# Kernel tuning notes

Hardware: AMD Instinct MI355X
Metric: run time of the kernel (lower is better)

Reference implementation:

```python
import jax, jax.numpy as jnp
import numpy as np

N_NODES = 50000
N_EDGES = 800000
HEADS = 2
HID = 64
NEG_SLOPE = 0.2


def setup_inputs() -> dict:
    key = jax.random.key(0)
    ks = jax.random.split(key, 8)
    x = jax.random.normal(ks[0], (N_NODES, 128), dtype=jnp.float32)
    W_src = jax.random.normal(ks[1], (128, HEADS * HID), dtype=jnp.float32) * (1.0 / np.sqrt(128))
    W_dst = jax.random.normal(ks[2], (128, HEADS * HID), dtype=jnp.float32) * (1.0 / np.sqrt(128))
    att_src = jax.random.normal(ks[3], (HEADS, HID), dtype=jnp.float32) * 0.1
    att_dst = jax.random.normal(ks[4], (HEADS, HID), dtype=jnp.float32) * 0.1
    bias = jax.random.normal(ks[5], (HEADS * HID,), dtype=jnp.float32) * 0.01
    prelu_w = jnp.full((HEADS * HID,), 0.25, dtype=jnp.float32)
    edge_index = jax.random.randint(ks[6], (2, N_EDGES), 0, N_NODES, dtype=jnp.int64)
    return {"x": x, "W_src": W_src, "W_dst": W_dst, "att_src": att_src,
            "att_dst": att_dst, "bias": bias, "prelu_w": prelu_w,
            "edge_index": edge_index}


def gat_prelu(x, W_src, W_dst, att_src, att_dst, bias, prelu_w, edge_index):
    N = x.shape[0]
    src, dst = edge_index[0], edge_index[1]
    xs = (x @ W_src).reshape(N, HEADS, HID)   # [N,H,C]
    xd = (x @ W_dst).reshape(N, HEADS, HID)
    a_src = jnp.einsum('nhc,hc->nh', xs, att_src)  # [N,H]
    a_dst = jnp.einsum('nhc,hc->nh', xd, att_dst)
    e = jax.nn.leaky_relu(a_src[src] + a_dst[dst], NEG_SLOPE)  # [E,H]
    # segment softmax over incoming edges of each dst node
    m = jax.ops.segment_max(e, dst, num_segments=N)            # [N,H]
    ee = jnp.exp(e - m[dst])
    denom = jax.ops.segment_sum(ee, dst, num_segments=N)
    alpha = ee / (denom[dst] + 1e-16)                          # [E,H]
    msg = xs[src] * alpha[:, :, None]                          # [E,H,C]
    out = jax.ops.segment_sum(msg, dst, num_segments=N)        # [N,H,C]
    out = out.reshape(N, HEADS * HID) + bias
    return jnp.where(out >= 0, out, prelu_w * out)


def reference(x, W_src, W_dst, att_src, att_dst, bias, prelu_w, edge_index):
    return gat_prelu(x, W_src, W_dst, att_src, att_dst, bias, prelu_w, edge_index)
```

## Files before the change

kernel.cpp:

```cpp
#include <hip/hip_runtime.h>
#include <hip/hip_fp16.h>


#define N_NODES 50000
#define N_EDGES 800000
#define CAP     56
#define BSH     8
#define NB      196
#define CHUNK   4096
#define NBLK    196
#define CCAP    64

#define OFF_A      0
#define OFF_CNT    800000
#define OFF_XS     1000256
#define OFF_BKT    13800256
#define OFF_SWZ    36200256
#define DOUT_COARSE 0
#define DOUT_CELL   19668992

typedef _Float16 f16x8 __attribute__((ext_vector_type(8)));
typedef float    f32x4 __attribute__((ext_vector_type(4)));
typedef unsigned long long u64;

__global__ __launch_bounds__(256) void k0_prep(
    const float* __restrict__ Wsrc, const float* __restrict__ Wdst,
    const float* __restrict__ att_s, const float* __restrict__ att_d,
    __half* __restrict__ swz)
{
    __shared__ float vS[128 * 4];
    const int nt = blockIdx.x;
    const int t = threadIdx.x;
    if (nt == 8) {
        if (t < 128) {
            const float* wsp = Wsrc + t * 128;
            const float* wdp = Wdst + t * 128;
            float a0 = 0.f, a1 = 0.f, a2 = 0.f, a3 = 0.f;
#pragma unroll 8
            for (int c = 0; c < 64; ++c) {
                a0 += wsp[c]      * att_s[c];
                a1 += wsp[64 + c] * att_s[64 + c];
                a2 += wdp[c]      * att_d[c];
                a3 += wdp[64 + c] * att_d[64 + c];
            }
            *(float4*)(vS + t * 4) = make_float4(a0, a1, a2, a3);
        }
        __syncthreads();
    }
    const int kb = t >> 6, L = t & 63;
    const int col = L & 15;
    const int krow = kb * 32 + ((L >> 4) & 3) * 8;
    f16x8 v;
    if (nt < 8) {
#pragma unroll
        for (int j = 0; j < 8; ++j)
            v[j] = (_Float16)Wsrc[(size_t)(krow + j) * 128 + nt * 16 + col];
    } else {
#pragma unroll
        for (int j = 0; j < 8; ++j)
            v[j] = (col < 4) ? (_Float16)vS[(krow + j) * 4 + col] : (_Float16)0.f;
    }
    *(f16x8*)(swz + ((size_t)(kb * 9 + nt) * 64 + L) * 8) = v;
}

__global__ __launch_bounds__(256) void k1_gemm(
    const float* __restrict__ x, const __half* __restrict__ swz,
    __half* __restrict__ xs, float* __restrict__ a_all)
{
    __shared__ __half tile[64 * 136];
    const int t = threadIdx.x;
    const int w = t >> 6, L = t & 63;
    const int m = L & 15, q = L >> 4;
    const int n_a = blockIdx.x * 64 + w * 16 + m;
    const int rrow = (n_a < N_NODES) ? n_a : (N_NODES - 1);
    const float* xrow = x + (size_t)rrow * 128;

    f32x4 acc[9];
#pragma unroll
    for (int nt = 0; nt < 9; ++nt) acc[nt] = (f32x4){0.f, 0.f, 0.f, 0.f};

#pragma unroll
    for (int kb = 0; kb < 4; ++kb) {
        const int k0 = kb * 32 + q * 8;
        float4 xa = *(const float4*)(xrow + k0);
        float4 xb = *(const float4*)(xrow + k0 + 4);
        f16x8 a;
        a[0] = (_Float16)xa.x; a[1] = (_Float16)xa.y;
        a[2] = (_Float16)xa.z; a[3] = (_Float16)xa.w;
        a[4] = (_Float16)xb.x; a[5] = (_Float16)xb.y;
        a[6] = (_Float16)xb.z; a[7] = (_Float16)xb.w;
        const f16x8* bbase = (const f16x8*)swz + (size_t)(kb * 9) * 64 + L;
#pragma unroll
        for (int nt = 0; nt < 9; ++nt) {
            f16x8 b = bbase[(size_t)nt * 64];
            acc[nt] = __builtin_amdgcn_mfma_f32_16x16x32_f16(a, b, acc[nt], 0, 0, 0);
        }
    }

    const int rloc = w * 16 + q * 4;
#pragma unroll
    for (int nt = 0; nt < 8; ++nt) {
#pragma unroll
        for (int r = 0; r < 4; ++r)
            tile[(rloc + r) * 136 + nt * 16 + m] = (__half)acc[nt][r];
    }
    __syncthreads();
    const int n0 = blockIdx.x * 64;
#pragma unroll
    for (int cc = 0; cc < 4; ++cc) {
        int task = cc * 256 + t;
        int row = task >> 4, ch = (task & 15) * 8;
        int n = n0 + row;
        if (n < N_NODES) {
            ulonglong2 v = *(const ulonglong2*)(tile + row * 136 + ch);
            *(ulonglong2*)(xs + (size_t)n * 128 + ch) = v;
        }
    }

    if (m < 4) {
#pragma unroll
        for (int r = 0; r < 4; ++r) {
            int n = n0 + rloc + r;
            if (n < N_NODES) a_all[(size_t)n * 4 + m] = acc[8][r];
        }
    }
}

__global__ __launch_bounds__(256) void kB_bin(
    const int* __restrict__ ei, const float* __restrict__ a_all,
    u64* __restrict__ coarse, int* __restrict__ cellcnt)
{
    __shared__ int lcnt[NB];
    const int t = threadIdx.x;
    if (t < NB) lcnt[t] = 0;
    __syncthreads();
    const int e0 = blockIdx.x * CHUNK;
#pragma unroll
    for (int u = 0; u < 8; ++u) {
        int e = e0 + u * 512 + t * 2;
        if (e < N_EDGES) {
            int2 ss = *(const int2*)(ei + e);
            int2 dd = *(const int2*)(ei + N_EDGES + e);
            float2 as0 = *(const float2*)(a_all + (size_t)ss.x * 4);
            float2 ad0 = *(const float2*)(a_all + (size_t)dd.x * 4 + 2);
            float2 as1 = *(const float2*)(a_all + (size_t)ss.y * 4);
            float2 ad1 = *(const float2*)(a_all + (size_t)dd.y * 4 + 2);
            float e00 = as0.x + ad0.x, e01 = as0.y + ad0.y;
            float e10 = as1.x + ad1.x, e11 = as1.y + ad1.y;
            e00 = (e00 >= 0.f) ? e00 : 0.2f * e00;
            e01 = (e01 >= 0.f) ? e01 : 0.2f * e01;
            e10 = (e10 >= 0.f) ? e10 : 0.2f * e10;
            e11 = (e11 >= 0.f) ? e11 : 0.2f * e11;
            __half2 hw0 = __floats2half2_rn(__expf(e00), __expf(e01));
            __half2 hw1 = __floats2half2_rn(__expf(e10), __expf(e11));
            unsigned lo0 = (unsigned)ss.x | ((unsigned)(dd.x & 255) << 16);
            unsigned lo1 = (unsigned)ss.y | ((unsigned)(dd.y & 255) << 16);
            u64 ent0 = (u64)lo0 | ((u64)*reinterpret_cast<unsigned*>(&hw0) << 32);
            u64 ent1 = (u64)lo1 | ((u64)*reinterpret_cast<unsigned*>(&hw1) << 32);
            int b0 = dd.x >> BSH, b1 = dd.y >> BSH;
            int p0 = atomicAdd(&lcnt[b0], 1);
            int p1 = atomicAdd(&lcnt[b1], 1);
            if (p0 < CCAP)
                coarse[((size_t)b0 * NBLK + blockIdx.x) * CCAP + p0] = ent0;
            if (p1 < CCAP)
                coarse[((size_t)b1 * NBLK + blockIdx.x) * CCAP + p1] = ent1;
        }
    }
    __syncthreads();
    if (t < NB) {
        int c = lcnt[t];
        cellcnt[t * NBLK + blockIdx.x] = (c < CCAP) ? c : CCAP;
    }
}

__global__ __launch_bounds__(512) void kD_fine(
    const u64* __restrict__ coarse, const int* __restrict__ cellcnt,
    int* __restrict__ cnt, int2* __restrict__ bkt)
{
    __shared__ int cur[256];
    __shared__ int ccnt[NBLK];
    const int b = blockIdx.x, t = threadIdx.x;
    if (t < 256) cur[t] = 0;
    if (t < NBLK) ccnt[t] = cellcnt[b * NBLK + t];
    __syncthreads();
    const u64* src = coarse + (size_t)b * NBLK * CCAP;
    const int HALF = CCAP / 2;
    for (int g2 = t; g2 < NBLK * HALF; g2 += 512) {
        int c = g2 >> 5, sp = (g2 & 31) * 2;
        int cc = ccnt[c];
        if (sp < cc) {
            ulonglong2 pr = *(const ulonglong2*)(src + (size_t)c * CCAP + sp);
            {
                unsigned lo = (unsigned)pr.x;
                int drel = (lo >> 16) & 255;
                int pos = atomicAdd(&cur[drel], 1);
                if (pos < CAP) {
                    int d = (b << BSH) + drel;
                    bkt[(size_t)d * CAP + pos] =
                        make_int2((int)(lo & 0xFFFF), (int)(unsigned)(pr.x >> 32));
                }
            }
            if (sp + 1 < cc) {
                unsigned lo = (unsigned)pr.y;
                int drel = (lo >> 16) & 255;
                int pos = atomicAdd(&cur[drel], 1);
                if (pos < CAP) {
                    int d = (b << BSH) + drel;
                    bkt[(size_t)d * CAP + pos] =
                        make_int2((int)(lo & 0xFFFF), (int)(unsigned)(pr.y >> 32));
                }
            }
        }
    }
    __syncthreads();
    if (t < 256) {
        int d = (b << BSH) + t;
        if (d < N_NODES) cnt[d] = cur[t];
    }
}

template<bool GUARD>
__device__ __forceinline__ void step8(const int2* __restrict__ row, int k, int m,
                                      int sh, int j, const __half* __restrict__ xs,
                                      float& ax, float& ay, float& sw)
{
    int4 p0 = *(const int4*)(row + k);
    int4 p1 = *(const int4*)(row + k + 2);
    int4 p2 = *(const int4*)(row + k + 4);
    int4 p3 = *(const int4*)(row + k + 6);
    int s0 = p0.x, s1 = p0.z, s2 = p1.x, s3 = p1.z;
    int s4 = p2.x, s5 = p2.z, s6 = p3.x, s7 = p3.z;
    unsigned w0 = (unsigned)p0.y, w1 = (unsigned)p0.w;
    unsigned w2 = (unsigned)p1.y, w3 = (unsigned)p1.w;
    unsigned w4 = (unsigned)p2.y, w5 = (unsigned)p2.w;
    unsigned w6 = (unsigned)p3.y, w7 = (unsigned)p3.w;
    if (GUARD) {
        if (k + 0 >= m) { s0 = 0; w0 = 0; }
        if (k + 1 >= m) { s1 = 0; w1 = 0; }
        if (k + 2 >= m) { s2 = 0; w2 = 0; }
        if (k + 3 >= m) { s3 = 0; w3 = 0; }
        if (k + 4 >= m) { s4 = 0; w4 = 0; }
        if (k + 5 >= m) { s5 = 0; w5 = 0; }
        if (k + 6 >= m) { s6 = 0; w6 = 0; }
        if (k + 7 >= m) { s7 = 0; w7 = 0; }
    }
    __half2 h0 = *(const __half2*)(xs + (size_t)s0 * 128 + j);
    __half2 h1 = *(const __half2*)(xs + (size_t)s1 * 128 + j);
    __half2 h2 = *(const __half2*)(xs + (size_t)s2 * 128 + j);
    __half2 h3 = *(const __half2*)(xs + (size_t)s3 * 128 + j);
    __half2 h4 = *(const __half2*)(xs + (size_t)s4 * 128 + j);
    __half2 h5 = *(const __half2*)(xs + (size_t)s5 * 128 + j);
    __half2 h6 = *(const __half2*)(xs + (size_t)s6 * 128 + j);
    __half2 h7 = *(const __half2*)(xs + (size_t)s7 * 128 + j);
    float a0 = __half2float(__ushort_as_half((unsigned short)(w0 >> sh)));
    float a1 = __half2float(__ushort_as_half((unsigned short)(w1 >> sh)));
    float a2 = __half2float(__ushort_as_half((unsigned short)(w2 >> sh)));
    float a3 = __half2float(__ushort_as_half((unsigned short)(w3 >> sh)));
    float a4 = __half2float(__ushort_as_half((unsigned short)(w4 >> sh)));
    float a5 = __half2float(__ushort_as_half((unsigned short)(w5 >> sh)));
    float a6 = __half2float(__ushort_as_half((unsigned short)(w6 >> sh)));
    float a7 = __half2float(__ushort_as_half((unsigned short)(w7 >> sh)));
    ax += __half2float(h0.x) * a0; ay += __half2float(h0.y) * a0;
    ax += __half2float(h1.x) * a1; ay += __half2float(h1.y) * a1;
    ax += __half2float(h2.x) * a2; ay += __half2float(h2.y) * a2;
    ax += __half2float(h3.x) * a3; ay += __half2float(h3.y) * a3;
    ax += __half2float(h4.x) * a4; ay += __half2float(h4.y) * a4;
    ax += __half2float(h5.x) * a5; ay += __half2float(h5.y) * a5;
    ax += __half2float(h6.x) * a6; ay += __half2float(h6.y) * a6;
    ax += __half2float(h7.x) * a7; ay += __half2float(h7.y) * a7;
    sw += ((a0 + a1) + (a2 + a3)) + ((a4 + a5) + (a6 + a7));
}

__global__ __launch_bounds__(256) void k6_agg(
    const int2* __restrict__ bkt, const int* __restrict__ cnt,
    const __half* __restrict__ xs, const float* __restrict__ bias,
    const float* __restrict__ prelu_w, float* __restrict__ out)
{
    const int n = blockIdx.x * 4 + (threadIdx.x >> 6);
    const int lane = threadIdx.x & 63;
    const int j = lane * 2;
    const int sh = (lane >> 5) * 16;
    int m = cnt[n]; if (m > CAP) m = CAP;
    const int2* row = bkt + (size_t)n * CAP;
    float ax = 0.f, ay = 0.f, sw = 0.f;
    int k = 0;
    for (; k + 8 <= m; k += 8)
        step8<false>(row, k, m, sh, j, xs, ax, ay, sw);
    if (k < m)
        step8<true>(row, k, m, sh, j, xs, ax, ay, sw);

    float inv = 1.f / (sw + 1e-16f);
    float o0 = ax * inv + bias[j];
    float o1 = ay * inv + bias[j + 1];
    float2 r;
    r.x = (o0 >= 0.f) ? o0 : prelu_w[j] * o0;
    r.y = (o1 >= 0.f) ? o1 : prelu_w[j + 1] * o1;
    *(float2*)(out + (size_t)n * 128 + j) = r;
}

extern "C" void kernel_launch(void* const* d_in, const int* in_sizes, int n_in,
                              void* d_out, int out_size, void* d_ws, size_t ws_size,
                              hipStream_t stream) {
    const float* x      = (const float*)d_in[0];
    const float* Wsrc   = (const float*)d_in[1];
    const float* Wdst   = (const float*)d_in[2];
    const float* att_s  = (const float*)d_in[3];
    const float* att_d  = (const float*)d_in[4];
    const float* bias   = (const float*)d_in[5];
    const float* prelu  = (const float*)d_in[6];
    const int*   ei     = (const int*)d_in[7];
    float* out = (float*)d_out;

    char* ws = (char*)d_ws;
    float*  a_all  = (float*)(ws + OFF_A);
    int*    cnt    = (int*)(ws + OFF_CNT);
    __half* xs     = (__half*)(ws + OFF_XS);
    int2*   bkt    = (int2*)(ws + OFF_BKT);
    __half* swz    = (__half*)(ws + OFF_SWZ);

    char* outb = (char*)d_out;
    u64* coarse  = (u64*)(outb + DOUT_COARSE);
    int* cellcnt = (int*)(outb + DOUT_CELL);

    k0_prep<<<9, 256, 0, stream>>>(Wsrc, Wdst, att_s, att_d, swz);
    k1_gemm<<<(N_NODES + 63) / 64, 256, 0, stream>>>(x, swz, xs, a_all);
    kB_bin<<<NBLK, 256, 0, stream>>>(ei, a_all, coarse, cellcnt);
    kD_fine<<<NB, 512, 0, stream>>>(coarse, cellcnt, cnt, bkt);
    k6_agg<<<N_NODES / 4, 256, 0, stream>>>(bkt, cnt, xs, bias, prelu, out);
}
```

Before: 169.4 us.

## Fuse fine binning into aggregation using per-block shared-memory buckets

Merges the fine bucketing kernel and the aggregation kernel into one. Each block handles half of a 256-node coarse bin, scatters that bin's edges into a shared-memory bucket list, then aggregates 16 nodes per wavefront straight from LDS. This removes the global bkt/cnt write and re-read plus one launch. In exchange each coarse bin is read twice, once by each half-block. The kernel uses about 57KB of LDS per block and only 392 blocks, so occupancy and parallelism drop.

```diff
diff --git a/kernel.cpp b/kernel.cpp
--- a/kernel.cpp
+++ b/kernel.cpp
@@ -12,12 +12,10 @@
 #define CCAP    64
 
 #define OFF_A      0
-#define OFF_CNT    800000
+#define OFF_CELL   800000
 #define OFF_XS     1000256
-#define OFF_BKT    13800256
+#define OFF_COARSE 13800256
 #define OFF_SWZ    36200256
-#define DOUT_COARSE 0
-#define DOUT_CELL   19668992
 
 typedef _Float16 f16x8 __attribute__((ext_vector_type(8)));
 typedef float    f32x4 __attribute__((ext_vector_type(4)));
@@ -173,52 +171,6 @@
     }
 }
 
-__global__ __launch_bounds__(512) void kD_fine(
-    const u64* __restrict__ coarse, const int* __restrict__ cellcnt,
-    int* __restrict__ cnt, int2* __restrict__ bkt)
-{
-    __shared__ int cur[256];
-    __shared__ int ccnt[NBLK];
-    const int b = blockIdx.x, t = threadIdx.x;
-    if (t < 256) cur[t] = 0;
-    if (t < NBLK) ccnt[t] = cellcnt[b * NBLK + t];
-    __syncthreads();
-    const u64* src = coarse + (size_t)b * NBLK * CCAP;
-    const int HALF = CCAP / 2;
-    for (int g2 = t; g2 < NBLK * HALF; g2 += 512) {
-        int c = g2 >> 5, sp = (g2 & 31) * 2;
-        int cc = ccnt[c];
-        if (sp < cc) {
-            ulonglong2 pr = *(const ulonglong2*)(src + (size_t)c * CCAP + sp);
-            {
-                unsigned lo = (unsigned)pr.x;
-                int drel = (lo >> 16) & 255;
-                int pos = atomicAdd(&cur[drel], 1);
-                if (pos < CAP) {
-                    int d = (b << BSH) + drel;
-                    bkt[(size_t)d * CAP + pos] =
-                        make_int2((int)(lo & 0xFFFF), (int)(unsigned)(pr.x >> 32));
-                }
-            }
-            if (sp + 1 < cc) {
-                unsigned lo = (unsigned)pr.y;
-                int drel = (lo >> 16) & 255;
-                int pos = atomicAdd(&cur[drel], 1);
-                if (pos < CAP) {
-                    int d = (b << BSH) + drel;
-                    bkt[(size_t)d * CAP + pos] =
-                        make_int2((int)(lo & 0xFFFF), (int)(unsigned)(pr.y >> 32));
-                }
-            }
-        }
-    }
-    __syncthreads();
-    if (t < 256) {
-        int d = (b << BSH) + t;
-        if (d < N_NODES) cnt[d] = cur[t];
-    }
-}
-
 template<bool GUARD>
 __device__ __forceinline__ void step8(const int2* __restrict__ row, int k, int m,
                                       int sh, int j, const __half* __restrict__ xs,
@@ -271,31 +223,80 @@
     sw += ((a0 + a1) + (a2 + a3)) + ((a4 + a5) + (a6 + a7));
 }
 
-__global__ __launch_bounds__(256) void k6_agg(
-    const int2* __restrict__ bkt, const int* __restrict__ cnt,
+__global__ __launch_bounds__(512, 4) void k5_binagg(
+    const u64* __restrict__ coarse, const int* __restrict__ cellcnt,
     const __half* __restrict__ xs, const float* __restrict__ bias,
     const float* __restrict__ prelu_w, float* __restrict__ out)
 {
-    const int n = blockIdx.x * 4 + (threadIdx.x >> 6);
-    const int lane = threadIdx.x & 63;
+    __shared__ __align__(16) int2 bl[128 * CAP];
+    __shared__ int cur[128];
+    __shared__ int ccnt[NBLK];
+    const int t = threadIdx.x;
+    const int b = blockIdx.x >> 1;
+    const int hi = (blockIdx.x & 1) << 7;
+    if (t < 128) cur[t] = 0;
+    if (t < NBLK) ccnt[t] = cellcnt[b * NBLK + t];
+    __syncthreads();
+
+    const u64* src = coarse + (size_t)b * NBLK * CCAP;
+    const int HALF = CCAP / 2;
+    for (int g2 = t; g2 < NBLK * HALF; g2 += 512) {
+        int c = g2 >> 5, sp = (g2 & 31) * 2;
+        int cc = ccnt[c];
+        if (sp < cc) {
+            ulonglong2 pr = *(const ulonglong2*)(src + (size_t)c * CCAP + sp);
+            {
+                unsigned lo = (unsigned)pr.x;
+                int drel = (lo >> 16) & 255;
+                if ((drel & 128) == hi) {
+                    int rel = drel & 127;
+                    int pos = atomicAdd(&cur[rel], 1);
+                    if (pos < CAP)
+                        bl[rel * CAP + pos] =
+                            make_int2((int)(lo & 0xFFFF), (int)(unsigned)(pr.x >> 32));
+                }
+            }
+            if (sp + 1 < cc) {
+                unsigned lo = (unsigned)pr.y;
+                int drel = (lo >> 16) & 255;
+                if ((drel & 128) == hi) {
+                    int rel = drel & 127;
+                    int pos = atomicAdd(&cur[rel], 1);
+                    if (pos < CAP)
+                        bl[rel * CAP + pos] =
+                            make_int2((int)(lo & 0xFFFF), (int)(unsigned)(pr.y >> 32));
+                }
+            }
+        }
+    }
+    __syncthreads();
+
+    const int w = t >> 6, lane = t & 63;
     const int j = lane * 2;
     const int sh = (lane >> 5) * 16;
-    int m = cnt[n]; if (m > CAP) m = CAP;
-    const int2* row = bkt + (size_t)n * CAP;
-    float ax = 0.f, ay = 0.f, sw = 0.f;
-    int k = 0;
-    for (; k + 8 <= m; k += 8)
-        step8<false>(row, k, m, sh, j, xs, ax, ay, sw);
-    if (k < m)
-        step8<true>(row, k, m, sh, j, xs, ax, ay, sw);
-
-    float inv = 1.f / (sw + 1e-16f);
-    float o0 = ax * inv + bias[j];
-    float o1 = ay * inv + bias[j + 1];
-    float2 r;
-    r.x = (o0 >= 0.f) ? o0 : prelu_w[j] * o0;
-    r.y = (o1 >= 0.f) ? o1 : prelu_w[j + 1] * o1;
-    *(float2*)(out + (size_t)n * 128 + j) = r;
+    const float bj0 = bias[j], bj1 = bias[j + 1];
+    const float pj0 = prelu_w[j], pj1 = prelu_w[j + 1];
+#pragma unroll 1
+    for (int i = 0; i < 16; ++i) {
+        const int rel = w * 16 + i;
+        const int d = (b << BSH) + hi + rel;
+        if (d >= N_NODES) break;
+        int m = cur[rel]; if (m > CAP) m = CAP;
+        const int2* row = bl + rel * CAP;
+        float ax = 0.f, ay = 0.f, sw = 0.f;
+        int k = 0;
+        for (; k + 8 <= m; k += 8)
+            step8<false>(row, k, m, sh, j, xs, ax, ay, sw);
+        if (k < m)
+            step8<true>(row, k, m, sh, j, xs, ax, ay, sw);
+        float inv = 1.f / (sw + 1e-16f);
+        float o0 = ax * inv + bj0;
+        float o1 = ay * inv + bj1;
+        float2 r;
+        r.x = (o0 >= 0.f) ? o0 : pj0 * o0;
+        r.y = (o1 >= 0.f) ? o1 : pj1 * o1;
+        *(float2*)(out + (size_t)d * 128 + j) = r;
+    }
 }
 
 extern "C" void kernel_launch(void* const* d_in, const int* in_sizes, int n_in,
@@ -312,19 +313,14 @@
     float* out = (float*)d_out;
 
     char* ws = (char*)d_ws;
-    float*  a_all  = (float*)(ws + OFF_A);
-    int*    cnt    = (int*)(ws + OFF_CNT);
-    __half* xs     = (__half*)(ws + OFF_XS);
-    int2*   bkt    = (int2*)(ws + OFF_BKT);
-    __half* swz    = (__half*)(ws + OFF_SWZ);
-
-    char* outb = (char*)d_out;
-    u64* coarse  = (u64*)(outb + DOUT_COARSE);
-    int* cellcnt = (int*)(outb + DOUT_CELL);
+    float*  a_all   = (float*)(ws + OFF_A);
+    int*    cellcnt = (int*)(ws + OFF_CELL);
+    __half* xs      = (__half*)(ws + OFF_XS);
+    u64*    coarse  = (u64*)(ws + OFF_COARSE);
+    __half* swz     = (__half*)(ws + OFF_SWZ);
 
     k0_prep<<<9, 256, 0, stream>>>(Wsrc, Wdst, att_s, att_d, swz);
     k1_gemm<<<(N_NODES + 63) / 64, 256, 0, stream>>>(x, swz, xs, a_all);
     kB_bin<<<NBLK, 256, 0, stream>>>(ei, a_all, coarse, cellcnt);
-    kD_fine<<<NB, 512, 0, stream>>>(coarse, cellcnt, cnt, bkt);
-    k6_agg<<<N_NODES / 4, 256, 0, stream>>>(bkt, cnt, xs, bias, prelu, out);
-}
+    k5_binagg<<<NB * 2, 512, 0, stream>>>(coarse, cellcnt, xs, bias, prelu, out);
+}
```

Result: no change. 167.2 us (-1.3%).

## Split aggregation into four column-pass blocks with 16 lanes per node

Applied to the files above, without the earlier changes.

The aggregation kernel now gives each node a quarter-wavefront of 16 lanes covering 32 output columns. Four separate blocks (passes) handle the four column slices of the same 16 nodes. The per-edge gather unroll drops from 8 to 4. The aim is to shrink each wave's working set and spread the gathers over more blocks and nodes for better memory-level parallelism. In exchange, every pass rereads the bucket rows, so bucket traffic grows fourfold, and each gathered xs row segment is only 64 bytes.

```diff
diff --git a/kernel.cpp b/kernel.cpp
--- a/kernel.cpp
+++ b/kernel.cpp
@@ -220,82 +220,68 @@
 }
 
 template<bool GUARD>
-__device__ __forceinline__ void step8(const int2* __restrict__ row, int k, int m,
-                                      int sh, int j, const __half* __restrict__ xs,
-                                      float& ax, float& ay, float& sw)
+__device__ __forceinline__ void pstep4(const int2* __restrict__ row, int k, int m,
+                                       int sh, int j, const __half* __restrict__ xs,
+                                       float& ax, float& ay, float& sw)
 {
     int4 p0 = *(const int4*)(row + k);
     int4 p1 = *(const int4*)(row + k + 2);
-    int4 p2 = *(const int4*)(row + k + 4);
-    int4 p3 = *(const int4*)(row + k + 6);
     int s0 = p0.x, s1 = p0.z, s2 = p1.x, s3 = p1.z;
-    int s4 = p2.x, s5 = p2.z, s6 = p3.x, s7 = p3.z;
     unsigned w0 = (unsigned)p0.y, w1 = (unsigned)p0.w;
     unsigned w2 = (unsigned)p1.y, w3 = (unsigned)p1.w;
-    unsigned w4 = (unsigned)p2.y, w5 = (unsigned)p2.w;
-    unsigned w6 = (unsigned)p3.y, w7 = (unsigned)p3.w;
     if (GUARD) {
         if (k + 0 >= m) { s0 = 0; w0 = 0; }
         if (k + 1 >= m) { s1 = 0; w1 = 0; }
         if (k + 2 >= m) { s2 = 0; w2 = 0; }
         if (k + 3 >= m) { s3 = 0; w3 = 0; }
-        if (k + 4 >= m) { s4 = 0; w4 = 0; }
-        if (k + 5 >= m) { s5 = 0; w5 = 0; }
-        if (k + 6 >= m) { s6 = 0; w6 = 0; }
-        if (k + 7 >= m) { s7 = 0; w7 = 0; }
     }
     __half2 h0 = *(const __half2*)(xs + (size_t)s0 * 128 + j);
     __half2 h1 = *(const __half2*)(xs + (size_t)s1 * 128 + j);
     __half2 h2 = *(const __half2*)(xs + (size_t)s2 * 128 + j);
     __half2 h3 = *(const __half2*)(xs + (size_t)s3 * 128 + j);
-    __half2 h4 = *(const __half2*)(xs + (size_t)s4 * 128 + j);
-    __half2 h5 = *(const __half2*)(xs + (size_t)s5 * 128 + j);
-    __half2 h6 = *(const __half2*)(xs + (size_t)s6 * 128 + j);
-    __half2 h7 = *(const __half2*)(xs + (size_t)s7 * 128 + j);
     float a0 = __half2float(__ushort_as_half((unsigned short)(w0 >> sh)));
     float a1 = __half2float(__ushort_as_half((unsigned short)(w1 >> sh)));
     float a2 = __half2float(__ushort_as_half((unsigned short)(w2 >> sh)));
     float a3 = __half2float(__ushort_as_half((unsigned short)(w3 >> sh)));
-    float a4 = __half2float(__ushort_as_half((unsigned short)(w4 >> sh)));
-    float a5 = __half2float(__ushort_as_half((unsigned short)(w5 >> sh)));
-    float a6 = __half2float(__ushort_as_half((unsigned short)(w6 >> sh)));
-    float a7 = __half2float(__ushort_as_half((unsigned short)(w7 >> sh)));
     ax += __half2float(h0.x) * a0; ay += __half2float(h0.y) * a0;
     ax += __half2float(h1.x) * a1; ay += __half2float(h1.y) * a1;
     ax += __half2float(h2.x) * a2; ay += __half2float(h2.y) * a2;
     ax += __half2float(h3.x) * a3; ay += __half2float(h3.y) * a3;
-    ax += __half2float(h4.x) * a4; ay += __half2float(h4.y) * a4;
-    ax += __half2float(h5.x) * a5; ay += __half2float(h5.y) * a5;
-    ax += __half2float(h6.x) * a6; ay += __half2float(h6.y) * a6;
-    ax += __half2float(h7.x) * a7; ay += __half2float(h7.y) * a7;
-    sw += ((a0 + a1) + (a2 + a3)) + ((a4 + a5) + (a6 + a7));
-}
-
-__global__ __launch_bounds__(256) void k6_agg(
+    sw += (a0 + a1) + (a2 + a3);
+}
+
+__global__ __launch_bounds__(256) void k6_pass(
     const int2* __restrict__ bkt, const int* __restrict__ cnt,
     const __half* __restrict__ xs, const float* __restrict__ bias,
     const float* __restrict__ prelu_w, float* __restrict__ out)
 {
-    const int n = blockIdx.x * 4 + (threadIdx.x >> 6);
-    const int lane = threadIdx.x & 63;
-    const int j = lane * 2;
-    const int sh = (lane >> 5) * 16;
-    int m = cnt[n]; if (m > CAP) m = CAP;
-    const int2* row = bkt + (size_t)n * CAP;
+    const int pass = blockIdx.x & 3;
+    const int grp  = blockIdx.x >> 2;
+    const int t = threadIdx.x;
+    const int w = t >> 6, lane = t & 63;
+    const int q = lane >> 4, l16 = lane & 15;
+    const int node = grp * 16 + w * 4 + q;
+    const int j = pass * 32 + l16 * 2;
+    const int sh = (pass & 2) ? 16 : 0;
+    int m = 0;
+    if (node < N_NODES) { m = cnt[node]; if (m > CAP) m = CAP; }
+    const int2* row = bkt + (size_t)node * CAP;
     float ax = 0.f, ay = 0.f, sw = 0.f;
     int k = 0;
-    for (; k + 8 <= m; k += 8)
-        step8<false>(row, k, m, sh, j, xs, ax, ay, sw);
+    for (; k + 4 <= m; k += 4)
+        pstep4<false>(row, k, m, sh, j, xs, ax, ay, sw);
     if (k < m)
-        step8<true>(row, k, m, sh, j, xs, ax, ay, sw);
-
-    float inv = 1.f / (sw + 1e-16f);
-    float o0 = ax * inv + bias[j];
-    float o1 = ay * inv + bias[j + 1];
-    float2 r;
-    r.x = (o0 >= 0.f) ? o0 : prelu_w[j] * o0;
-    r.y = (o1 >= 0.f) ? o1 : prelu_w[j + 1] * o1;
-    *(float2*)(out + (size_t)n * 128 + j) = r;
+        pstep4<true>(row, k, m, sh, j, xs, ax, ay, sw);
+
+    if (node < N_NODES) {
+        float inv = 1.f / (sw + 1e-16f);
+        float o0 = ax * inv + bias[j];
+        float o1 = ay * inv + bias[j + 1];
+        float2 r;
+        r.x = (o0 >= 0.f) ? o0 : prelu_w[j] * o0;
+        r.y = (o1 >= 0.f) ? o1 : prelu_w[j + 1] * o1;
+        *(float2*)(out + (size_t)node * 128 + j) = r;
+    }
 }
 
 extern "C" void kernel_launch(void* const* d_in, const int* in_sizes, int n_in,
@@ -326,5 +312,5 @@
     k1_gemm<<<(N_NODES + 63) / 64, 256, 0, stream>>>(x, swz, xs, a_all);
     kB_bin<<<NBLK, 256, 0, stream>>>(ei, a_all, coarse, cellcnt);
     kD_fine<<<NB, 512, 0, stream>>>(coarse, cellcnt, cnt, bkt);
-    k6_agg<<<N_NODES / 4, 256, 0, stream>>>(bkt, cnt, xs, bias, prelu, out);
-}
+    k6_pass<<<4 * ((N_NODES + 15) / 16), 256, 0, stream>>>(bkt, cnt, xs, bias, prelu, out);
+}
```

Result: slower. 181.2 us (+6.9%).
